# Kernel tuning notes

Measured on AMD Instinct MI355X. Metric: run time of the kernel, lower is better.

The kernel has to match this reference:

```python
import jax, jax.numpy as jnp
import numpy as np

N_NODES = 100000
N_EDGES = 1200000
D = 64
GCN_LAYERS = 2
KEEP_PROB = 0.7


def setup_inputs() -> dict:
    key = jax.random.key(0)
    k1, k2, k3, k4, k5, k6, k7 = jax.random.split(key, 7)
    all_emb = jax.random.normal(k1, (N_NODES, D), dtype=jnp.float32)
    W = jax.random.normal(k2, (D, D), dtype=jnp.float32) * 0.05
    b = jax.random.normal(k3, (D,), dtype=jnp.float32) * 0.05
    # sparse adjacency values (e.g. normalized weights)
    vals = jax.random.uniform(k4, (N_EDGES,), dtype=jnp.float32)
    # per-layer dropout uniforms, mirrors torch.rand(len(values)) each layer
    drop_u = jax.random.uniform(k5, (GCN_LAYERS, N_EDGES), dtype=jnp.float32)
    rows = jax.random.randint(k6, (N_EDGES,), 0, N_NODES)
    cols = jax.random.randint(k7, (N_EDGES,), 0, N_NODES)
    return {"all_emb": all_emb, "W": W, "b": b, "vals": vals,
            "drop_u": drop_u, "rows": rows, "cols": cols}


def reference(all_emb, W, b, vals, drop_u, rows, cols):
    # emb[0] = fc(all_emb)
    acc = all_emb @ W.T + b  # [N, D]
    x = all_emb
    for layer in range(GCN_LAYERS):
        # edge dropout: keep iff (u + keep_prob) floors to 1, scale by 1/keep_prob
        keep = (drop_u[layer] + KEEP_PROB) >= 1.0
        v = jnp.where(keep, vals / KEEP_PROB, 0.0)  # [E]
        # SpMM: x <- A_dropped @ x via gather + segment-sum scatter
        msgs = v[:, None] * x[cols]  # [E, D]
        x = jax.ops.segment_sum(msgs, rows, num_segments=N_NODES)  # [N, D]
        acc = acc + x
    # mean over stacked (gcn_layers + 1) embeddings
    return acc / float(GCN_LAYERS + 1)
```

## Files before the change

### kernel.cpp

```cpp
#include <hip/hip_runtime.h>

#define N_NODES 100000
#define N_EDGES 1200000
#define D 64
#define KEEP_PROB 0.7f
#define INV_KEEP (1.0f / KEEP_PROB)
#define NBUCK 1564
#define MAXB 1024
#define PPART 256
#define CHUNK4 1172

#define ALOAD_I(p)   __hip_atomic_load((p), __ATOMIC_RELAXED, __HIP_MEMORY_SCOPE_AGENT)
#define ALOAD_U64(p) __hip_atomic_load((p), __ATOMIC_RELAXED, __HIP_MEMORY_SCOPE_AGENT)

__global__ __launch_bounds__(256) void zero_kernel(float4* __restrict__ p, int n4) {
    int i = blockIdx.x * 256 + threadIdx.x;
    if (i < n4) p[i] = make_float4(0.f, 0.f, 0.f, 0.f);
}
__global__ __launch_bounds__(256) void zero_ints_kernel(int* __restrict__ p, int n) {
    int i = blockIdx.x * 256 + threadIdx.x;
    if (i < n) p[i] = 0;
}

__global__ __launch_bounds__(256) void bucket_hist_kernel(const int4* __restrict__ rows4,
                                                          int* __restrict__ bcnt,
                                                          int* __restrict__ h) {
    __shared__ int hh[NBUCK];
    int p = blockIdx.x;
    int t = threadIdx.x;
    for (int i = t; i < NBUCK; i += 256) hh[i] = 0;
    __syncthreads();
    int i0 = p * CHUNK4;
    int i1 = i0 + CHUNK4;
    if (i1 > N_EDGES / 4) i1 = N_EDGES / 4;
    for (int i = i0 + t; i < i1; i += 256) {
        int4 r = rows4[i];
        atomicAdd(&hh[r.x >> 6], 1);
        atomicAdd(&hh[r.y >> 6], 1);
        atomicAdd(&hh[r.z >> 6], 1);
        atomicAdd(&hh[r.w >> 6], 1);
    }
    __syncthreads();
    int* hp = h + p * NBUCK;
    for (int i = t; i < NBUCK; i += 256) {
        int c = hh[i];
        hp[i] = c;
        if (c) atomicAdd(&bcnt[i << 4], c);
    }
}

__global__ __launch_bounds__(256) void bucket_scan_kernel(const int* __restrict__ bcnt,
                                                          int* __restrict__ bbase,
                                                          int* __restrict__ Pstart) {
    __shared__ int part[256];
    const int CH = 7;
    int t = threadIdx.x;
    int e[CH]; int s = 0;
    #pragma unroll
    for (int k = 0; k < CH; ++k) {
        int j = t * CH + k;
        e[k] = (j < NBUCK) ? ALOAD_I(&bcnt[j << 4]) : 0;
        s += e[k];
    }
    part[t] = s;
    __syncthreads();
    for (int d = 1; d < 256; d <<= 1) {
        int w = (t >= d) ? part[t - d] : 0;
        __syncthreads();
        part[t] += w;
        __syncthreads();
    }
    int run = part[t] - s;
    #pragma unroll
    for (int k = 0; k < CH; ++k) {
        int j = t * CH + k;
        if (j < NBUCK) { bbase[j] = run; run += e[k]; }
    }
    if (t == 255) bbase[NBUCK] = run;
    if (t == 0)   Pstart[N_NODES] = N_EDGES;
}

__global__ __launch_bounds__(256) void rebase_kernel(int* __restrict__ h,
                                                     const int* __restrict__ bbase) {
    int b = blockIdx.x * 256 + threadIdx.x;
    if (b >= NBUCK) return;
    int run = bbase[b];
    for (int p = 0; p < PPART; ++p) {
        int idx = p * NBUCK + b;
        int c = h[idx];
        h[idx] = run;
        run += c;
    }
}

__global__ __launch_bounds__(256) void partition_kernel(
    const int4*   __restrict__ rows4,
    const int4*   __restrict__ cols4,
    const float4* __restrict__ vals4,
    const float4* __restrict__ u04,
    const float4* __restrict__ u14,
    const int*    __restrict__ h,
    uint4*        __restrict__ edata) {
    __shared__ int cur[NBUCK];
    int p = blockIdx.x;
    int t = threadIdx.x;
    const int* hp = h + p * NBUCK;
    for (int i = t; i < NBUCK; i += 256) cur[i] = hp[i];
    __syncthreads();

    int i0 = p * CHUNK4;
    int i1 = i0 + CHUNK4;
    if (i1 > N_EDGES / 4) i1 = N_EDGES / 4;
    for (int i = i0 + t; i < i1; i += 256) {
        int4   r  = rows4[i];
        int4   c  = cols4[i];
        float4 v  = vals4[i];
        float4 u0 = u04[i];
        float4 u1 = u14[i];

        int p0 = atomicAdd(&cur[r.x >> 6], 1);
        int p1 = atomicAdd(&cur[r.y >> 6], 1);
        int p2 = atomicAdd(&cur[r.z >> 6], 1);
        int p3 = atomicAdd(&cur[r.w >> 6], 1);

        uint4 rec; float vv;
        vv = v.x * INV_KEEP;
        rec.x = (unsigned)c.x;
        rec.y = __float_as_uint((u0.x + KEEP_PROB >= 1.0f) ? vv : 0.f);
        rec.z = __float_as_uint((u1.x + KEEP_PROB >= 1.0f) ? vv : 0.f);
        rec.w = (unsigned)r.x;
        edata[p0] = rec;
        vv = v.y * INV_KEEP;
        rec.x = (unsigned)c.y;
        rec.y = __float_as_uint((u0.y + KEEP_PROB >= 1.0f) ? vv : 0.f);
        rec.z = __float_as_uint((u1.y + KEEP_PROB >= 1.0f) ? vv : 0.f);
        rec.w = (unsigned)r.y;
        edata[p1] = rec;
        vv = v.z * INV_KEEP;
        rec.x = (unsigned)c.z;
        rec.y = __float_as_uint((u0.z + KEEP_PROB >= 1.0f) ? vv : 0.f);
        rec.z = __float_as_uint((u1.z + KEEP_PROB >= 1.0f) ? vv : 0.f);
        rec.w = (unsigned)r.z;
        edata[p2] = rec;
        vv = v.w * INV_KEEP;
        rec.x = (unsigned)c.w;
        rec.y = __float_as_uint((u0.w + KEEP_PROB >= 1.0f) ? vv : 0.f);
        rec.z = __float_as_uint((u1.w + KEEP_PROB >= 1.0f) ? vv : 0.f);
        rec.w = (unsigned)r.w;
        edata[p3] = rec;
    }
}

__global__ __launch_bounds__(256) void finalize_kernel(
    uint4* __restrict__ edata,
    const int* __restrict__ bbase,
    int*   __restrict__ Pstart,
    uint4* __restrict__ scratch) {
    __shared__ uint4 recs[MAXB];
    __shared__ int cnt[64], cur[64], part[64];
    int b = blockIdx.x;
    int t = threadIdx.x;
    int base = bbase[b];
    int size = bbase[b + 1] - base;
    int row0 = b << 6;
    bool small = (size <= MAXB);

    const unsigned long long* src = (const unsigned long long*)(edata + base);
    if (small) {
        for (int i = t; i < size; i += 256) {
            unsigned long long lo = ALOAD_U64(src + 2 * i);
            unsigned long long hi = ALOAD_U64(src + 2 * i + 1);
            uint4 r;
            r.x = (unsigned)lo; r.y = (unsigned)(lo >> 32);
            r.z = (unsigned)hi; r.w = (unsigned)(hi >> 32);
            recs[i] = r;
        }
    } else {
        unsigned long long* dst = (unsigned long long*)(scratch + base);
        for (int i = t; i < 2 * size; i += 256) dst[i] = ALOAD_U64(src + i);
    }
    if (t < 64) cnt[t] = 0;
    __syncthreads();

    const uint4* gsrc = scratch + base;
    for (int i = t; i < size; i += 256) {
        unsigned rw = small ? recs[i].w : gsrc[i].w;
        atomicAdd(&cnt[rw & 63], 1);
    }
    __syncthreads();

    int v = (t < 64) ? cnt[t] : 0;
    if (t < 64) part[t] = v;
    __syncthreads();
    for (int d = 1; d < 64; d <<= 1) {
        int w = (t >= d && t < 64) ? part[t - d] : 0;
        __syncthreads();
        if (t < 64) part[t] += w;
        __syncthreads();
    }
    int R = N_NODES - row0; if (R > 64) R = 64;
    if (t < 64) {
        int pref = part[t] - v;
        cur[t] = pref;
        if (t < R) Pstart[row0 + t] = base + pref;
    }
    __syncthreads();

    for (int i = t; i < size; i += 256) {
        uint4 r = small ? recs[i] : gsrc[i];
        int lr = (int)(r.w & 63);
        int slot = atomicAdd(&cur[lr], 1);
        uint4 outrec;
        outrec.x = r.x; outrec.y = r.y;
        outrec.z = r.x; outrec.w = r.z;
        edata[base + slot] = outrec;
    }
}

__global__ __launch_bounds__(256) void spmm_gather_kernel(
    const float4* __restrict__ x_in,
    const unsigned long long* __restrict__ edata,
    const int*   __restrict__ Pstart,
    float4*      __restrict__ io,
    int layer) {
    int tid = blockIdx.x * 256 + threadIdx.x;
    int row = tid >> 4;
    int l16 = threadIdx.x & 15;
    if (row >= N_NODES) return;
    int start = ALOAD_I(&Pstart[row]);
    int end   = ALOAD_I(&Pstart[row + 1]);
    float4 acc = make_float4(0.f, 0.f, 0.f, 0.f);
    #pragma unroll 8
    for (int i = start; i < end; ++i) {
        unsigned long long rec = ALOAD_U64(&edata[2 * i + layer]);
        int   c = (int)(rec & 0xffffffffu);
        float v = __uint_as_float((unsigned)(rec >> 32));
        int  cc = (v != 0.f) ? c : 0;
        float4 x = x_in[(cc << 4) + l16];
        acc.x = fmaf(v, x.x, acc.x);
        acc.y = fmaf(v, x.y, acc.y);
        acc.z = fmaf(v, x.z, acc.z);
        acc.w = fmaf(v, x.w, acc.w);
    }
    int o = (row << 4) + l16;
    if (layer == 0) {
        io[o] = acc;
    } else {
        float4 p = io[o];
        p.x = (p.x + acc.x) * (1.0f / 3.0f);
        p.y = (p.y + acc.y) * (1.0f / 3.0f);
        p.z = (p.z + acc.z) * (1.0f / 3.0f);
        p.w = (p.w + acc.w) * (1.0f / 3.0f);
        io[o] = p;
    }
}

__global__ __launch_bounds__(256) void fc_add_kernel(
    const float* __restrict__ emb,
    const float* __restrict__ W,
    const float* __restrict__ b,
    const float* __restrict__ x1,
    float*       __restrict__ out) {
    __shared__ float Ws[D * 65];
    __shared__ float Es[4 * D];

    int t = threadIdx.x;
    #pragma unroll
    for (int i = 0; i < 16; ++i) {
        int idx = i * 256 + t;
        Ws[(idx >> 6) * 65 + (idx & 63)] = W[idx];
    }
    int node0 = blockIdx.x * 4;
    Es[t] = emb[node0 * D + t];
    __syncthreads();

    int local = t >> 6;
    int j     = t & 63;
    int n     = node0 + local;

    float acc = b[j];
    const float* es = &Es[local * D];
    const float* ws = &Ws[j * 65];
    #pragma unroll
    for (int k = 0; k < D; ++k) acc += es[k] * ws[k];
    out[n * D + j] = acc + x1[n * D + j];
}

__global__ __launch_bounds__(256) void spmm_atomic_kernel(
    const float* __restrict__ x_in,
    const float* __restrict__ vals,
    const float* __restrict__ drop_u,
    const int*   __restrict__ rows,
    const int*   __restrict__ cols,
    float*       __restrict__ x_out) {
    int wave = (blockIdx.x * 256 + threadIdx.x) >> 6;
    int lane = threadIdx.x & 63;
    if (wave >= N_EDGES) return;
    float u = drop_u[wave];
    if (u + KEEP_PROB < 1.0f) return;
    float v = vals[wave] * INV_KEEP;
    atomicAdd(&x_out[rows[wave] * D + lane], v * x_in[cols[wave] * D + lane]);
}

__global__ __launch_bounds__(256) void scale_kernel(float4* __restrict__ p, int n4) {
    int i = blockIdx.x * 256 + threadIdx.x;
    if (i < n4) {
        float4 v = p[i];
        v.x *= (1.f/3.f); v.y *= (1.f/3.f); v.z *= (1.f/3.f); v.w *= (1.f/3.f);
        p[i] = v;
    }
}

extern "C" void kernel_launch(void* const* d_in, const int* in_sizes, int n_in,
                              void* d_out, int out_size, void* d_ws, size_t ws_size,
                              hipStream_t stream) {
    const float* all_emb = (const float*)d_in[0];
    const float* W       = (const float*)d_in[1];
    const float* b       = (const float*)d_in[2];
    const float* vals    = (const float*)d_in[3];
    const float* drop_u  = (const float*)d_in[4];
    const int*   rows    = (const int*)d_in[5];
    const int*   cols    = (const int*)d_in[6];

    float* out = (float*)d_out;

    char* ws = (char*)d_ws;
    float* x1     = (float*)(ws);
    int*   Pstart = (int*)  (ws + 25600000);
    uint4* edata  = (uint4*)(ws + 26000064);
    int*   bcnt   = (int*)  (ws + 45200064);
    int*   bbase  = (int*)  (ws + 45300160);
    int*   h      = (int*)  (ws + 19200000);
    const size_t WS_NEEDED = 45406528;

    const int n4 = N_NODES * D / 4;
    const int zb = (n4 + 255) / 256;
    const int gather_blocks = (N_NODES * 16 + 255) / 256;

    if (ws_size >= WS_NEEDED) {
        zero_ints_kernel<<<(NBUCK * 16 + 255) / 256, 256, 0, stream>>>(bcnt, NBUCK * 16);
        bucket_hist_kernel<<<PPART, 256, 0, stream>>>((const int4*)rows, bcnt, h);
        bucket_scan_kernel<<<1, 256, 0, stream>>>(bcnt, bbase, Pstart);
        rebase_kernel<<<(NBUCK + 255) / 256, 256, 0, stream>>>(h, bbase);
        partition_kernel<<<PPART, 256, 0, stream>>>(
            (const int4*)rows, (const int4*)cols, (const float4*)vals,
            (const float4*)drop_u, (const float4*)(drop_u + N_EDGES),
            h, edata);
        finalize_kernel<<<NBUCK, 256, 0, stream>>>(edata, bbase, Pstart, (uint4*)x1);
        spmm_gather_kernel<<<gather_blocks, 256, 0, stream>>>(
            (const float4*)all_emb, (const unsigned long long*)edata, Pstart,
            (float4*)x1, 0);
        fc_add_kernel<<<N_NODES / 4, 256, 0, stream>>>(all_emb, W, b, x1, out);
        spmm_gather_kernel<<<gather_blocks, 256, 0, stream>>>(
            (const float4*)x1, (const unsigned long long*)edata, Pstart,
            (float4*)out, 1);
    } else {
        const int spmm_blocks = (N_EDGES + 3) / 4;
        zero_kernel<<<zb, 256, 0, stream>>>((float4*)x1, n4);
        spmm_atomic_kernel<<<spmm_blocks, 256, 0, stream>>>(all_emb, vals, drop_u,
                                                            rows, cols, x1);
        fc_add_kernel<<<N_NODES / 4, 256, 0, stream>>>(all_emb, W, b, x1, out);
        spmm_atomic_kernel<<<spmm_blocks, 256, 0, stream>>>(x1, vals,
                                                            drop_u + N_EDGES,
                                                            rows, cols, out);
        scale_kernel<<<zb, 256, 0, stream>>>((float4*)out, n4);
    }
}
```

Measured before the change: 310.8 us.

## Register-tile fc_add kernel over 64 nodes per block with float4 LDS reads

```diff
diff --git a/kernel.cpp b/kernel.cpp
--- a/kernel.cpp
+++ b/kernel.cpp
@@ -255,35 +255,79 @@
     }
 }
 
+#define FMA4(A, E, WV) \
+    A.x = fmaf(E, WV.x, A.x); A.y = fmaf(E, WV.y, A.y); \
+    A.z = fmaf(E, WV.z, A.z); A.w = fmaf(E, WV.w, A.w);
+
 __global__ __launch_bounds__(256) void fc_add_kernel(
     const float* __restrict__ emb,
     const float* __restrict__ W,
     const float* __restrict__ b,
     const float* __restrict__ x1,
     float*       __restrict__ out) {
-    __shared__ float Ws[D * 65];
-    __shared__ float Es[4 * D];
+    __shared__ float Wt[D * 68];
+    __shared__ float Es[64 * 68];
 
     int t = threadIdx.x;
+    int n0 = blockIdx.x * 64;
+
     #pragma unroll
     for (int i = 0; i < 16; ++i) {
         int idx = i * 256 + t;
-        Ws[(idx >> 6) * 65 + (idx & 63)] = W[idx];
-    }
-    int node0 = blockIdx.x * 4;
-    Es[t] = emb[node0 * D + t];
-    __syncthreads();
-
-    int local = t >> 6;
-    int j     = t & 63;
-    int n     = node0 + local;
-
-    float acc = b[j];
-    const float* es = &Es[local * D];
-    const float* ws = &Ws[j * 65];
-    #pragma unroll
-    for (int k = 0; k < D; ++k) acc += es[k] * ws[k];
-    out[n * D + j] = acc + x1[n * D + j];
+        Wt[(idx & 63) * 68 + (idx >> 6)] = W[idx];
+    }
+    #pragma unroll
+    for (int i = 0; i < 4; ++i) {
+        int idx4 = i * 256 + t;
+        int n = idx4 >> 4;
+        int k0 = (idx4 & 15) * 4;
+        float4 v = make_float4(0.f, 0.f, 0.f, 0.f);
+        if (n0 + n < N_NODES) v = *(const float4*)&emb[(n0 + n) * D + k0];
+        *(float4*)&Es[n * 68 + k0] = v;
+    }
+    __syncthreads();
+
+    int tj = t & 15;
+    int tn = t >> 4;
+    int j0 = tj * 4;
+
+    float4 bb = *(const float4*)&b[j0];
+    float4 acc[4];
+    #pragma unroll
+    for (int i = 0; i < 4; ++i) acc[i] = bb;
+
+    const float* es = &Es[(tn * 4) * 68];
+    #pragma unroll
+    for (int kc = 0; kc < 16; ++kc) {
+        int k = kc * 4;
+        float4 w0 = *(const float4*)&Wt[(k + 0) * 68 + j0];
+        float4 w1 = *(const float4*)&Wt[(k + 1) * 68 + j0];
+        float4 w2 = *(const float4*)&Wt[(k + 2) * 68 + j0];
+        float4 w3 = *(const float4*)&Wt[(k + 3) * 68 + j0];
+        float4 e0 = *(const float4*)&es[0 * 68 + k];
+        float4 e1 = *(const float4*)&es[1 * 68 + k];
+        float4 e2 = *(const float4*)&es[2 * 68 + k];
+        float4 e3 = *(const float4*)&es[3 * 68 + k];
+        FMA4(acc[0], e0.x, w0); FMA4(acc[0], e0.y, w1);
+        FMA4(acc[0], e0.z, w2); FMA4(acc[0], e0.w, w3);
+        FMA4(acc[1], e1.x, w0); FMA4(acc[1], e1.y, w1);
+        FMA4(acc[1], e1.z, w2); FMA4(acc[1], e1.w, w3);
+        FMA4(acc[2], e2.x, w0); FMA4(acc[2], e2.y, w1);
+        FMA4(acc[2], e2.z, w2); FMA4(acc[2], e2.w, w3);
+        FMA4(acc[3], e3.x, w0); FMA4(acc[3], e3.y, w1);
+        FMA4(acc[3], e3.z, w2); FMA4(acc[3], e3.w, w3);
+    }
+
+    #pragma unroll
+    for (int i = 0; i < 4; ++i) {
+        int n = n0 + tn * 4 + i;
+        if (n < N_NODES) {
+            float4 p = *(const float4*)&x1[n * D + j0];
+            float4 a = acc[i];
+            a.x += p.x; a.y += p.y; a.z += p.z; a.w += p.w;
+            *(float4*)&out[n * D + j0] = a;
+        }
+    }
 }
 
 __global__ __launch_bounds__(256) void spmm_atomic_kernel(
@@ -336,6 +380,7 @@
     const int n4 = N_NODES * D / 4;
     const int zb = (n4 + 255) / 256;
     const int gather_blocks = (N_NODES * 16 + 255) / 256;
+    const int fc_blocks = (N_NODES + 63) / 64;
 
     if (ws_size >= WS_NEEDED) {
         zero_ints_kernel<<<(NBUCK * 16 + 255) / 256, 256, 0, stream>>>(bcnt, NBUCK * 16);
@@ -350,7 +395,7 @@
         spmm_gather_kernel<<<gather_blocks, 256, 0, stream>>>(
             (const float4*)all_emb, (const unsigned long long*)edata, Pstart,
             (float4*)x1, 0);
-        fc_add_kernel<<<N_NODES / 4, 256, 0, stream>>>(all_emb, W, b, x1, out);
+        fc_add_kernel<<<fc_blocks, 256, 0, stream>>>(all_emb, W, b, x1, out);
         spmm_gather_kernel<<<gather_blocks, 256, 0, stream>>>(
             (const float4*)x1, (const unsigned long long*)edata, Pstart,
             (float4*)out, 1);
@@ -359,7 +404,7 @@
         zero_kernel<<<zb, 256, 0, stream>>>((float4*)x1, n4);
         spmm_atomic_kernel<<<spmm_blocks, 256, 0, stream>>>(all_emb, vals, drop_u,
                                                             rows, cols, x1);
-        fc_add_kernel<<<N_NODES / 4, 256, 0, stream>>>(all_emb, W, b, x1, out);
+        fc_add_kernel<<<fc_blocks, 256, 0, stream>>>(all_emb, W, b, x1, out);
         spmm_atomic_kernel<<<spmm_blocks, 256, 0, stream>>>(x1, vals,
                                                             drop_u + N_EDGES,
                                                             rows, cols, out);
```

Measured after the change: 300.1 us. 3.4% less time.
